# Kernel tuning notes

Measured on AMD Instinct MI355X. Metric: run time of the kernel, lower is better.

Reference implementation:

```python
import jax, jax.numpy as jnp
import numpy as np

N_WIRES = 12
N_LAYERS = 3
DIM = 2 ** N_WIRES
BATCH = 512


def _rot_matrix(a, b, c):
    """Fused U = RZ(c) @ RY(b) @ RX(a) as a 2x2 complex64 matrix."""
    ca, sa = jnp.cos(a * 0.5), jnp.sin(a * 0.5)
    cb, sb = jnp.cos(b * 0.5), jnp.sin(b * 0.5)
    ec = jnp.exp(-0.5j * c)  # e^{-i c/2}
    zero = jnp.zeros_like(ec)
    RX = jnp.stack([jnp.stack([ca + 0j, -1j * sa]),
                    jnp.stack([-1j * sa, ca + 0j])]).astype(jnp.complex64)
    RY = jnp.stack([jnp.stack([cb, -sb]),
                    jnp.stack([sb, cb])]).astype(jnp.complex64)
    RZ = jnp.stack([jnp.stack([ec, zero]),
                    jnp.stack([zero, jnp.conj(ec)])]).astype(jnp.complex64)
    return RZ @ RY @ RX


def _apply_1q(psi, U, wire):
    B = psi.shape[0]
    dl, dr = 2 ** wire, 2 ** (N_WIRES - wire - 1)
    s = psi.reshape(B, dl, 2, dr)
    s = jnp.einsum('ij,bljr->blir', U, s)
    return s.reshape(B, DIM)


def _apply_cnot_adjacent(psi, wire):
    # CNOT(control=wire, target=wire+1): permute (10 <-> 11) on the joint axis
    B = psi.shape[0]
    dl, dr = 2 ** wire, 2 ** (N_WIRES - wire - 2)
    s = psi.reshape(B, dl, 4, dr)
    s = jnp.take(s, jnp.array([0, 1, 3, 2]), axis=2)
    return s.reshape(B, DIM)


def _circuit(state_batch, weights):
    psi = state_batch.astype(jnp.complex64)  # QubitStateVector init
    for l in range(N_LAYERS):
        for w in range(N_WIRES):
            U = _rot_matrix(weights[l, w, 0], weights[l, w, 1], weights[l, w, 2])
            psi = _apply_1q(psi, U, w)
        for w in range(N_WIRES - 1):  # 'cnot' chain entanglement
            psi = _apply_cnot_adjacent(psi, w)
    B = state_batch.shape[0]
    probs = (psi.real ** 2 + psi.imag ** 2).reshape((B,) + (2,) * N_WIRES)
    feats = []
    for w in range(N_WIRES):  # <Z_w> = p(0) - p(1)
        axes = tuple(a for a in range(1, N_WIRES + 1) if a != w + 1)
        p = probs.sum(axis=axes)  # (B, 2)
        feats.append(p[:, 0] - p[:, 1])
    return jnp.stack(feats, axis=-1)  # (B, N_WIRES)


def setup_inputs() -> dict:
    key = jax.random.key(0)
    k1, k2, k3, k4 = jax.random.split(key, 4)
    state = jax.random.normal(k1, (BATCH, DIM), dtype=jnp.float32)
    state = state / jnp.linalg.norm(state, axis=-1, keepdims=True)  # valid quantum states
    weights = jax.random.uniform(k2, (N_LAYERS, N_WIRES, 3), dtype=jnp.float32,
                                 minval=0.0, maxval=2.0 * np.pi)
    head_w = jax.random.normal(k3, (1, N_WIRES), dtype=jnp.float32) / np.sqrt(N_WIRES)
    head_b = jax.random.normal(k4, (1,), dtype=jnp.float32) * 0.01
    return {"state_batch": state, "weights": weights, "head_w": head_w, "head_b": head_b}


def reference(state_batch, weights, head_w, head_b):
    feats = _circuit(state_batch, weights)          # (B, N_WIRES) PauliZ expvals
    out = feats @ head_w.T + head_b                 # Linear(num_wires, 1)
    return out[:, 0]                                # squeeze(-1) -> (B,)
```

## Files before the change

kernel.cpp:

```cpp
#include <hip/hip_runtime.h>


namespace {

typedef float v2f __attribute__((ext_vector_type(2)));

constexpr int N_WIRES  = 12;
constexpr int DIM      = 1 << N_WIRES;
constexpr int THREADS  = 256;
constexpr int PER      = 16;
constexpr int NGATES   = 36;
constexpr int PADC     = 4606;

__device__ __forceinline__ v2f cmul(v2f u, v2f p) {
    v2f d;
    asm("v_pk_mul_f32 %0, %1, %2 op_sel_hi:[1,0]"
        : "=v"(d) : "v"(p), "v"(u));
    asm("v_pk_fma_f32 %0, %1, %2, %0 op_sel:[1,1,0] op_sel_hi:[0,1,1] neg_lo:[0,1,0]"
        : "+v"(d) : "v"(p), "v"(u));
    return d;
}
__device__ __forceinline__ void cfma(v2f& d, v2f u, v2f p) {
    asm("v_pk_fma_f32 %0, %1, %2, %0 op_sel_hi:[1,0,1]"
        : "+v"(d) : "v"(p), "v"(u));
    asm("v_pk_fma_f32 %0, %1, %2, %0 op_sel:[1,1,0] op_sel_hi:[0,1,1] neg_lo:[0,1,0]"
        : "+v"(d) : "v"(p), "v"(u));
}

__device__ __forceinline__ void apply4(v2f amp[PER], const v2f (*Um)[4], int gbase)
{
    #pragma unroll
    for (int gg = 0; gg < 4; ++gg) {
        const v2f u00 = Um[gbase + gg][0];
        const v2f u01 = Um[gbase + gg][1];
        const v2f u10 = Um[gbase + gg][2];
        const v2f u11 = Um[gbase + gg][3];
        const int st = 8 >> gg;
        #pragma unroll
        for (int k0 = 0; k0 < PER; ++k0) {
            if (k0 & st) continue;
            const int k1 = k0 | st;
            const v2f p = amp[k0], q = amp[k1];
            v2f np = cmul(u00, p); cfma(np, u01, q);
            v2f nq = cmul(u10, p); cfma(nq, u11, q);
            amp[k0] = np;
            amp[k1] = nq;
        }
    }
}

__global__ __launch_bounds__(THREADS, 2)
void qcirc_kernel(const float* __restrict__ state,
                  const float* __restrict__ weights,
                  const float* __restrict__ head_w,
                  const float* __restrict__ head_b,
                  float* __restrict__ out,
                  float* __restrict__ dbg)
{
    __shared__ __align__(16) v2f buf[2][PADC];
    __shared__ __align__(16) v2f Umat[NGATES][4];
    __shared__ float redbuf[THREADS / 64];

    const int t = threadIdx.x;
    const int b = blockIdx.x;

    if (t < NGATES) {
        const float* wp = weights + t * 3;
        float ha = 0.5f * wp[0], hb = 0.5f * wp[1], hc = 0.5f * wp[2];
        float ca = cosf(ha), sa = sinf(ha);
        float cb = cosf(hb), sb = sinf(hb);
        float ecr = cosf(hc), eci = -sinf(hc);
        float t0 = cb * ca, t1 = sb * sa, t2 = sb * ca, t3 = cb * sa;
        float u00r =  ecr * t0 - eci * t1;
        float u00i =  ecr * t1 + eci * t0;
        float u10r =  ecr * t2 - eci * t3;
        float u10i = -ecr * t3 - eci * t2;
        Umat[t][0] = (v2f){ u00r,  u00i};
        Umat[t][1] = (v2f){-u10r,  u10i};
        Umat[t][2] = (v2f){ u10r,  u10i};
        Umat[t][3] = (v2f){ u00r, -u00i};
    }

    const int T  = t >> 4, u = t & 15;
    const int bA = 18 * T + u;
    const int bB = 288 * T + u;
    const int bC = 18 * t;
    const int tb  = t ^ (t >> 1);
    const int tbx = tb ^ 128;
    const int pb0 = 18 * (tb  >> 4) + (tb  & 15);
    const int pb1 = 18 * (tbx >> 4) + (tbx & 15);

    float hw[N_WIRES];
    #pragma unroll
    for (int w = 0; w < N_WIRES; ++w) hw[w] = head_w[w];
    int it = t ^ (t >> 1); it ^= it >> 2; it ^= it >> 4;
    float chi = 0.f;
    #pragma unroll
    for (int w = 0; w < 8; ++w)
        chi += ((it >> (7 - w)) & 1) ? -hw[w] : hw[w];
    const int parfill = (__popc(t) & 1) ? 0xF : 0;

    v2f amp[PER];
    {
        const float* sp = state + (size_t)b * DIM;
        #pragma unroll
        for (int k = 0; k < PER; ++k)
            amp[k] = (v2f){sp[(k << 8) | t], 0.f};
    }
    __syncthreads();

    #pragma unroll 1
    for (int pass = 0; pass < 2; ++pass) {
        #pragma unroll
        for (int l = 0; l < 3; ++l) {
            const int gb = l * 12;
            if (l > 0) {
                const v2f* src = buf[(3 * l - 1) & 1];
                #pragma unroll
                for (int k = 0; k < PER; ++k) {
                    const int g = k ^ (k >> 1);
                    amp[k] = src[((k & 1) ? pb1 : pb0) + 288 * g];
                }
            }

            apply4(amp, Umat, gb + 0);
            {
                v2f* w = &buf[(3 * l) & 1][bA];
                #pragma unroll
                for (int k = 0; k < PER; ++k) w[288 * k] = amp[k];
            }
            __syncthreads();
            {
                const v2f* r = &buf[(3 * l) & 1][bB];
                #pragma unroll
                for (int k = 0; k < PER; ++k) amp[k] = r[18 * k];
            }

            apply4(amp, Umat, gb + 4);
            {
                v2f* w = &buf[(3 * l + 1) & 1][bB];
                #pragma unroll
                for (int k = 0; k < PER; ++k) w[18 * k] = amp[k];
            }
            __syncthreads();
            {
                const float4* r = reinterpret_cast<const float4*>(&buf[(3 * l + 1) & 1][bC]);
                #pragma unroll
                for (int k = 0; k < PER / 2; ++k) {
                    float4 v = r[k];
                    amp[2 * k]     = (v2f){v.x, v.y};
                    amp[2 * k + 1] = (v2f){v.z, v.w};
                }
            }

            apply4(amp, Umat, gb + 8);
            if (l < 2) {
                float4* w = reinterpret_cast<float4*>(&buf[(3 * l + 2) & 1][bC]);
                #pragma unroll
                for (int k = 0; k < PER / 2; ++k)
                    w[k] = make_float4(amp[2 * k].x, amp[2 * k].y,
                                       amp[2 * k + 1].x, amp[2 * k + 1].y);
                __syncthreads();
            }
        }

        float acc = 0.f;
        #pragma unroll
        for (int k = 0; k < PER; ++k) {
            int ml = (k ^ (k >> 1)); ml ^= ml >> 2; ml ^= parfill;
            float c = chi;
            c += ((ml >> 3) & 1) ? -hw[8]  : hw[8];
            c += ((ml >> 2) & 1) ? -hw[9]  : hw[9];
            c += ((ml >> 1) & 1) ? -hw[10] : hw[10];
            c += ( ml       & 1) ? -hw[11] : hw[11];
            float p = amp[k].x * amp[k].x + amp[k].y * amp[k].y;
            acc += p * c;
        }

        #pragma unroll
        for (int off = 32; off > 0; off >>= 1)
            acc += __shfl_down(acc, off, 64);
        if ((t & 63) == 0) redbuf[t >> 6] = acc;
        __syncthreads();
        if (t == 0) {
            float s = 0.f;
            #pragma unroll
            for (int q = 0; q < THREADS / 64; ++q) s += redbuf[q];
            s += head_b[0];
            if (pass == 0) out[b] = s;
            else           dbg[b] = s;
        }
    }
}

}

extern "C" void kernel_launch(void* const* d_in, const int* in_sizes, int n_in,
                              void* d_out, int out_size, void* d_ws, size_t ws_size,
                              hipStream_t stream)
{
    const float* state   = (const float*)d_in[0];
    const float* weights = (const float*)d_in[1];
    const float* head_w  = (const float*)d_in[2];
    const float* head_b  = (const float*)d_in[3];
    float* out = (float*)d_out;
    float* dbg = (float*)d_ws;

    const int batch = in_sizes[0] / DIM;
    qcirc_kernel<<<batch, THREADS, 0, stream>>>(state, weights, head_w, head_b,
                                                out, dbg);
}
```

Before: 91.49 us.

## Drop duplicate circuit pass, single-buffer shared memory, raise occupancy target

Removes the second full evaluation of the circuit that previously wrote a duplicate result into a workspace buffer, so each block simulates the circuit once. Collapses the double-buffered shared state into one buffer, adding a barrier after the cross-layer read to avoid overwriting data still being read. Raises the launch-bounds occupancy hint from 2 to 4 blocks per CU, which lets more blocks fit but may constrain registers for the 16-amplitude per-thread state.

Result: faster. 76.14 us (-16.8%).

```diff
diff --git a/kernel.cpp b/kernel.cpp
--- a/kernel.cpp
+++ b/kernel.cpp
@@ -49,15 +49,14 @@
     }
 }
 
-__global__ __launch_bounds__(THREADS, 2)
+__global__ __launch_bounds__(THREADS, 4)
 void qcirc_kernel(const float* __restrict__ state,
                   const float* __restrict__ weights,
                   const float* __restrict__ head_w,
                   const float* __restrict__ head_b,
-                  float* __restrict__ out,
-                  float* __restrict__ dbg)
+                  float* __restrict__ out)
 {
-    __shared__ __align__(16) v2f buf[2][PADC];
+    __shared__ __align__(16) v2f buf[PADC];
     __shared__ __align__(16) v2f Umat[NGATES][4];
     __shared__ float redbuf[THREADS / 64];
 
@@ -109,87 +108,73 @@
     }
     __syncthreads();
 
-    #pragma unroll 1
-    for (int pass = 0; pass < 2; ++pass) {
-        #pragma unroll
-        for (int l = 0; l < 3; ++l) {
-            const int gb = l * 12;
-            if (l > 0) {
-                const v2f* src = buf[(3 * l - 1) & 1];
-                #pragma unroll
-                for (int k = 0; k < PER; ++k) {
-                    const int g = k ^ (k >> 1);
-                    amp[k] = src[((k & 1) ? pb1 : pb0) + 288 * g];
-                }
-            }
-
-            apply4(amp, Umat, gb + 0);
-            {
-                v2f* w = &buf[(3 * l) & 1][bA];
-                #pragma unroll
-                for (int k = 0; k < PER; ++k) w[288 * k] = amp[k];
+    #pragma unroll
+    for (int l = 0; l < 3; ++l) {
+        const int gb = l * 12;
+        if (l > 0) {
+            #pragma unroll
+            for (int k = 0; k < PER; ++k) {
+                const int g = k ^ (k >> 1);
+                amp[k] = buf[((k & 1) ? pb1 : pb0) + 288 * g];
             }
             __syncthreads();
-            {
-                const v2f* r = &buf[(3 * l) & 1][bB];
-                #pragma unroll
-                for (int k = 0; k < PER; ++k) amp[k] = r[18 * k];
-            }
+        }
 
-            apply4(amp, Umat, gb + 4);
-            {
-                v2f* w = &buf[(3 * l + 1) & 1][bB];
-                #pragma unroll
-                for (int k = 0; k < PER; ++k) w[18 * k] = amp[k];
-            }
-            __syncthreads();
-            {
-                const float4* r = reinterpret_cast<const float4*>(&buf[(3 * l + 1) & 1][bC]);
-                #pragma unroll
-                for (int k = 0; k < PER / 2; ++k) {
-                    float4 v = r[k];
-                    amp[2 * k]     = (v2f){v.x, v.y};
-                    amp[2 * k + 1] = (v2f){v.z, v.w};
-                }
-            }
+        apply4(amp, Umat, gb + 0);
+        #pragma unroll
+        for (int k = 0; k < PER; ++k) buf[bA + 288 * k] = amp[k];
+        __syncthreads();
 
-            apply4(amp, Umat, gb + 8);
-            if (l < 2) {
-                float4* w = reinterpret_cast<float4*>(&buf[(3 * l + 2) & 1][bC]);
-                #pragma unroll
-                for (int k = 0; k < PER / 2; ++k)
-                    w[k] = make_float4(amp[2 * k].x, amp[2 * k].y,
-                                       amp[2 * k + 1].x, amp[2 * k + 1].y);
-                __syncthreads();
+        #pragma unroll
+        for (int k = 0; k < PER; ++k) amp[k] = buf[bB + 18 * k];
+        apply4(amp, Umat, gb + 4);
+        #pragma unroll
+        for (int k = 0; k < PER; ++k) buf[bB + 18 * k] = amp[k];
+        __syncthreads();
+
+        {
+            const float4* r = reinterpret_cast<const float4*>(&buf[bC]);
+            #pragma unroll
+            for (int k = 0; k < PER / 2; ++k) {
+                float4 v = r[k];
+                amp[2 * k]     = (v2f){v.x, v.y};
+                amp[2 * k + 1] = (v2f){v.z, v.w};
             }
         }
+        apply4(amp, Umat, gb + 8);
+        if (l < 2) {
+            float4* w = reinterpret_cast<float4*>(&buf[bC]);
+            #pragma unroll
+            for (int k = 0; k < PER / 2; ++k)
+                w[k] = make_float4(amp[2 * k].x, amp[2 * k].y,
+                                   amp[2 * k + 1].x, amp[2 * k + 1].y);
+            __syncthreads();
+        }
+    }
 
-        float acc = 0.f;
+    float acc = 0.f;
+    #pragma unroll
+    for (int k = 0; k < PER; ++k) {
+        int ml = (k ^ (k >> 1)); ml ^= ml >> 2; ml ^= parfill;
+        float c = chi;
+        c += ((ml >> 3) & 1) ? -hw[8]  : hw[8];
+        c += ((ml >> 2) & 1) ? -hw[9]  : hw[9];
+        c += ((ml >> 1) & 1) ? -hw[10] : hw[10];
+        c += ( ml       & 1) ? -hw[11] : hw[11];
+        float p = amp[k].x * amp[k].x + amp[k].y * amp[k].y;
+        acc += p * c;
+    }
+
+    #pragma unroll
+    for (int off = 32; off > 0; off >>= 1)
+        acc += __shfl_down(acc, off, 64);
+    if ((t & 63) == 0) redbuf[t >> 6] = acc;
+    __syncthreads();
+    if (t == 0) {
+        float s = 0.f;
         #pragma unroll
-        for (int k = 0; k < PER; ++k) {
-            int ml = (k ^ (k >> 1)); ml ^= ml >> 2; ml ^= parfill;
-            float c = chi;
-            c += ((ml >> 3) & 1) ? -hw[8]  : hw[8];
-            c += ((ml >> 2) & 1) ? -hw[9]  : hw[9];
-            c += ((ml >> 1) & 1) ? -hw[10] : hw[10];
-            c += ( ml       & 1) ? -hw[11] : hw[11];
-            float p = amp[k].x * amp[k].x + amp[k].y * amp[k].y;
-            acc += p * c;
-        }
-
-        #pragma unroll
-        for (int off = 32; off > 0; off >>= 1)
-            acc += __shfl_down(acc, off, 64);
-        if ((t & 63) == 0) redbuf[t >> 6] = acc;
-        __syncthreads();
-        if (t == 0) {
-            float s = 0.f;
-            #pragma unroll
-            for (int q = 0; q < THREADS / 64; ++q) s += redbuf[q];
-            s += head_b[0];
-            if (pass == 0) out[b] = s;
-            else           dbg[b] = s;
-        }
+        for (int q = 0; q < THREADS / 64; ++q) s += redbuf[q];
+        out[b] = s + head_b[0];
     }
 }
 
@@ -204,9 +189,7 @@
     const float* head_w  = (const float*)d_in[2];
     const float* head_b  = (const float*)d_in[3];
     float* out = (float*)d_out;
-    float* dbg = (float*)d_ws;
 
     const int batch = in_sizes[0] / DIM;
-    qcirc_kernel<<<batch, THREADS, 0, stream>>>(state, weights, head_w, head_b,
-                                                out, dbg);
+    qcirc_kernel<<<batch, THREADS, 0, stream>>>(state, weights, head_w, head_b, out);
 }
```
